# Performance work log

Hardware: AMD Instinct MI355X
Metric: run time of the kernel (lower is better)

Reference implementation:

```python
import jax, jax.numpy as jnp
import numpy as np

B, S, DIN, DH = 8, 4096, 1024, 1024


def setup_inputs() -> dict:
    key = jax.random.key(0)
    k1, k2, k3, k4 = jax.random.split(key, 4)
    x = jax.random.normal(k1, (B, S, DIN), jnp.float32)
    # previous hidden state must be strictly positive (log-domain scan)
    h = jax.random.uniform(k2, (B, 1, DH), jnp.float32, minval=0.05, maxval=0.95)
    W = jax.random.normal(k3, (2 * DH, DIN), jnp.float32) * (1.0 / np.sqrt(DIN))
    b = jax.random.normal(k4, (2 * DH,), jnp.float32) * 0.01
    return {"x": x, "h": h, "W": W, "b": b}


def _log_g(x):
    # log of g(x) = x + 0.5 if x >= 0 else sigmoid(x)
    return jnp.where(x >= 0, jnp.log(jnp.where(x >= 0, x, 0.0) + 0.5), -jax.nn.softplus(-x))


def reference(x, h, W, b):
    # gate/hidden projection: (B,S,2H)
    gh = jnp.einsum('bsi,oi->bso', x, W) + b
    gate, hidden = jnp.split(gh, 2, axis=2)  # each (B,S,H)

    # minGRU recurrence h_t = (1-z_t) h_{t-1} + z_t g(hidden_t), z_t = sigmoid(gate_t)
    # evaluated with the Heinsen log-space parallel scan
    log_z = -jax.nn.softplus(-gate)        # log sigmoid(gate)
    log_coeffs = -jax.nn.softplus(gate)    # log (1 - sigmoid(gate))
    log_h0 = jnp.log(h)                    # (B,1,H)
    log_values = jnp.concatenate([log_h0, log_z + _log_g(hidden)], axis=1)  # (B,S+1,H)

    a_star = jnp.cumsum(jnp.pad(log_coeffs, ((0, 0), (1, 0), (0, 0))), axis=1)  # (B,S+1,H)
    log_h = a_star + jax.lax.cumlogsumexp(log_values - a_star, axis=1)
    return jnp.exp(log_h)[:, 1:]  # (B,S,H)
```

## Files before the change

### kernel.cpp

```cpp
#include <hip/hip_runtime.h>

typedef __attribute__((ext_vector_type(4))) float f32x4;
typedef __attribute__((ext_vector_type(8))) short short8;

#define NCHUNK 64
#define CLEN 64

__device__ __forceinline__ unsigned short f2bf(float f) {
    union { float f; unsigned int u; } a; a.f = f;
    unsigned int r = a.u + 0x7fffu + ((a.u >> 16) & 1u);
    return (unsigned short)(r >> 16);
}
__device__ __forceinline__ float bf2f(unsigned short u) {
    union { unsigned int u; float f; } a; a.u = ((unsigned int)u) << 16;
    return a.f;
}

__global__ __launch_bounds__(256) void conv_all(const float* __restrict__ x,
                                                const float* __restrict__ W,
                                                unsigned short* __restrict__ xb,
                                                unsigned short* __restrict__ wbP) {
    int bid = blockIdx.x, t = threadIdx.x;
    if (bid < 2048) {
        for (int i = bid * 256 + t; i < 8388608; i += 524288) {
            float4 v = reinterpret_cast<const float4*>(x)[i];
            ushort4 o;
            o.x = f2bf(v.x); o.y = f2bf(v.y); o.z = f2bf(v.z); o.w = f2bf(v.w);
            reinterpret_cast<ushort4*>(xb)[i] = o;
        }
    } else {
        int base = (bid - 2048) * 256 + t;
#pragma unroll
        for (int k = 0; k < 4; ++k) {
            int i = base + k * 131072;
            int r = i >> 8, c4 = i & 255;
            float4 v = reinterpret_cast<const float4*>(W)[i];
            int rp;
            if (r < 1024) rp = (r >> 6) * 128 + (r & 63);
            else { int c = r - 1024; rp = (c >> 6) * 128 + 64 + (c & 63); }
            ushort4 o;
            o.x = f2bf(v.x); o.y = f2bf(v.y); o.z = f2bf(v.z); o.w = f2bf(v.w);
            reinterpret_cast<ushort4*>(wbP)[rp * 256 + c4] = o;
        }
    }
}

__global__ __launch_bounds__(256) void gemm_fused(
    const unsigned short* __restrict__ xb, const unsigned short* __restrict__ wbP,
    const float* __restrict__ bias,
    unsigned int* __restrict__ CVg, float* __restrict__ CCc, float* __restrict__ CVc)
{
    __shared__ unsigned short sm[16384];
    const int bid = blockIdx.x;
    const int swz = (bid & 7) * 512 + (bid >> 3);
    const int nt = swz & 15, mt = swz >> 4;
    const int m0 = mt * 128, chBase = nt * 64, n0p = nt * 128;
    const int t = threadIdx.x;
    const int w = t >> 6, l = t & 63;
    const int wr = (w >> 1) * 64, wc = (w & 1) * 64;

    const int srow = t >> 3;
    const int sblk = (t & 7) ^ (srow & 7);
    const unsigned short* gA = xb  + (size_t)(m0 + srow)  * 1024 + sblk * 8;
    const unsigned short* gB = wbP + (size_t)(n0p + srow) * 1024 + sblk * 8;

    f32x4 acc[4][4];
#pragma unroll
    for (int i = 0; i < 4; ++i)
#pragma unroll
        for (int j = 0; j < 4; ++j) acc[i][j] = (f32x4){0.f, 0.f, 0.f, 0.f};

    for (int kt = 0; kt < 16; ++kt) {
        __syncthreads();
        const unsigned short* a = gA + kt * 64;
        const unsigned short* b = gB + kt * 64;
#pragma unroll
        for (int j = 0; j < 4; ++j) {
            __builtin_amdgcn_global_load_lds(
                (const __attribute__((address_space(1))) unsigned int*)(a + j * 32768),
                (__attribute__((address_space(3))) unsigned int*)
                    ((__attribute__((address_space(3))) char*)sm + t * 16 + j * 4096), 16, 0, 0);
            __builtin_amdgcn_global_load_lds(
                (const __attribute__((address_space(1))) unsigned int*)(b + j * 32768),
                (__attribute__((address_space(3))) unsigned int*)
                    ((__attribute__((address_space(3))) char*)sm + 16384 + t * 16 + j * 4096), 16, 0, 0);
        }
        asm volatile("s_waitcnt vmcnt(0)" ::: "memory");
        __syncthreads();

#pragma unroll
        for (int ks = 0; ks < 2; ++ks) {
            short8 af[4], bfr[4];
#pragma unroll
            for (int mi = 0; mi < 4; ++mi) {
                int row = wr + mi * 16 + (l & 15);
                int slot = ((ks << 2) + (l >> 4)) ^ (l & 7);
                af[mi] = *reinterpret_cast<const short8*>((const char*)sm + row * 128 + slot * 16);
            }
#pragma unroll
            for (int ni = 0; ni < 4; ++ni) {
                int row = wc + ni * 16 + (l & 15);
                int slot = ((ks << 2) + (l >> 4)) ^ (l & 7);
                bfr[ni] = *reinterpret_cast<const short8*>((const char*)sm + 16384 + row * 128 + slot * 16);
            }
#pragma unroll
            for (int mi = 0; mi < 4; ++mi)
#pragma unroll
                for (int ni = 0; ni < 4; ++ni)
                    acc[mi][ni] = __builtin_amdgcn_mfma_f32_16x16x32_bf16(af[mi], bfr[ni], acc[mi][ni], 0, 0, 0);
        }
    }

    const bool isHid = (wc != 0);
    float bv[4];
#pragma unroll
    for (int ni = 0; ni < 4; ++ni) {
        int ch = chBase + ni * 16 + (l & 15);
        bv[ni] = bias[isHid ? (1024 + ch) : ch];
    }
    __syncthreads();
    {
        unsigned short* eb = sm + (w >> 1) * 8192 + (isHid ? 4096 : 0);
#pragma unroll
        for (int mi = 0; mi < 4; ++mi)
#pragma unroll
            for (int ni = 0; ni < 4; ++ni)
#pragma unroll
                for (int r = 0; r < 4; ++r) {
                    float v = acc[mi][ni][r] + bv[ni];
                    float o = isHid ? ((v >= 0.f) ? (v + 0.5f) : (1.f / (1.f + __expf(-v))))
                                    : (1.f / (1.f + __expf(-v)));
                    int row = mi * 16 + ((l >> 4) << 2) + r;
                    int ch = ni * 16 + (l & 15);
                    eb[row * 64 + ch] = f2bf(o);
                }
    }
    __syncthreads();
    {
        int chunk = t >> 7, tt = t & 127;
        const unsigned short* zb = sm + chunk * 8192;
        const unsigned short* gb = zb + 4096;
        int mrow0 = m0 + chunk * 64;
#pragma unroll 4
        for (int i = 0; i < 32; ++i) {
            int idx = i * 128 + tt;
            int row = idx >> 6, ch = idx & 63;
            float z = bf2f(zb[row * 64 + ch]);
            float gg = bf2f(gb[row * 64 + ch]);
            CVg[(size_t)(mrow0 + row) * 1024 + chBase + ch] =
                (unsigned int)f2bf(1.f - z) | ((unsigned int)f2bf(z * gg) << 16);
        }
        if (tt < 64) {
            float C = 1.f, V = 0.f;
#pragma unroll 8
            for (int i = 0; i < 64; ++i) {
                float z = bf2f(zb[i * 64 + tt]);
                float gg = bf2f(gb[i * 64 + tt]);
                float c = bf2f(f2bf(1.f - z));
                float vv = bf2f(f2bf(z * gg));
                C *= c; V = c * V + vv;
            }
            int b = mrow0 >> 12, ck = (mrow0 >> 6) & 63;
            CCc[(size_t)(b * 64 + ck) * 1024 + chBase + tt] = C;
            CVc[(size_t)(b * 64 + ck) * 1024 + chBase + tt] = V;
        }
    }
}

__global__ __launch_bounds__(256) void scan_prefix(
    const float* __restrict__ CC, const float* __restrict__ CV,
    const float* __restrict__ h0, float* __restrict__ Hinit)
{
    int g = blockIdx.x * 256 + threadIdx.x;
    int h = g & 1023, b = g >> 10;
    float hc = h0[b * 1024 + h];
#pragma unroll 8
    for (int ck = 0; ck < NCHUNK; ++ck) {
        int idx = (b * 64 + ck) * 1024 + h;
        Hinit[idx] = hc;
        hc = CC[idx] * hc + CV[idx];
    }
}

__global__ __launch_bounds__(256) void scan_apply(
    const unsigned int* __restrict__ CVg, const float* __restrict__ Hinit,
    float* __restrict__ out)
{
    int g = blockIdx.x * 256 + threadIdx.x;
    int ch = g & 1023, ck = (g >> 10) & 63, b = g >> 16;
    int mbase = b * 4096 + ck * CLEN;
    const unsigned int* pc = CVg + (size_t)mbase * 1024 + ch;
    float h = Hinit[g];
    float* po = out + (size_t)mbase * 1024 + ch;
#pragma unroll 8
    for (int i = 0; i < CLEN; ++i) {
        unsigned int u = pc[i * 1024];
        h = bf2f((unsigned short)(u & 0xffff)) * h + bf2f((unsigned short)(u >> 16));
        po[i * 1024] = h;
    }
}

extern "C" void kernel_launch(void* const* d_in, const int* in_sizes, int n_in,
                              void* d_out, int out_size, void* d_ws, size_t ws_size,
                              hipStream_t stream)
{
    const float* x    = (const float*)d_in[0];
    const float* h0   = (const float*)d_in[1];
    const float* W    = (const float*)d_in[2];
    const float* bias = (const float*)d_in[3];
    float* out = (float*)d_out;

    unsigned short* xb = (unsigned short*)d_out;
    unsigned short* wbP = (unsigned short*)d_ws;
    unsigned int* CVg = (unsigned int*)((char*)d_ws + 4194304);
    float* CCc   = (float*)((char*)d_ws + 138412032);
    float* CVc   = (float*)((char*)d_ws + 140509184);
    float* Hinit = (float*)((char*)d_ws + 142606336);

    conv_all<<<2560, 256, 0, stream>>>(x, W, xb, wbP);
    gemm_fused<<<4096, 256, 0, stream>>>(xb, wbP, bias, CVg, CCc, CVc);
    scan_prefix<<<32, 256, 0, stream>>>(CCc, CVc, h0, Hinit);
    scan_apply<<<2048, 256, 0, stream>>>(CVg, Hinit, out);
}
```

Before: 488.8 us.

## Triple-buffer GEMM K-loop with async LDS prefetch and fuse scan kernels

The GEMM main loop now uses a three-stage LDS ring with K-tiles of 32. The next-but-one tile is issued via global_load_lds while the current tile is consumed, with partial vmcnt waits and one barrier per iteration. MFMA issue is wrapped in setprio, which should overlap memory latency with compute instead of a full load-wait-compute cycle. Separately, the serial scan_prefix kernel is removed: each scan_all thread recomputes its chunk's initial state from the chunk carries. That saves a launch and the Hinit round trip, but adds redundant serial work for later chunks.

```diff
diff --git a/kernel.cpp b/kernel.cpp
--- a/kernel.cpp
+++ b/kernel.cpp
@@ -45,12 +45,26 @@
     }
 }
 
+
+#define GLOAD(SRC, DST) \
+    __builtin_amdgcn_global_load_lds((const __attribute__((address_space(1))) unsigned int*)(SRC), \
+        (__attribute__((address_space(3))) unsigned int*)(DST), 16, 0, 0)
+
+#define STAGE(KT, BUF) { \
+    const unsigned short* _a = gA + (KT) * 32; \
+    const unsigned short* _b = gB + (KT) * 32; \
+    char* _dA = lds + (BUF) * 8192 + t * 16; \
+    char* _dB = lds + 24576 + (BUF) * 8192 + t * 16; \
+    GLOAD(_a, _dA); GLOAD(_a + 65536, _dA + 4096); \
+    GLOAD(_b, _dB); GLOAD(_b + 65536, _dB + 4096); }
+
 __global__ __launch_bounds__(256) void gemm_fused(
     const unsigned short* __restrict__ xb, const unsigned short* __restrict__ wbP,
     const float* __restrict__ bias,
     unsigned int* __restrict__ CVg, float* __restrict__ CCc, float* __restrict__ CVc)
 {
-    __shared__ unsigned short sm[16384];
+    __shared__ char lds[49152];
+    unsigned short* sm = (unsigned short*)lds;
     const int bid = blockIdx.x;
     const int swz = (bid & 7) * 512 + (bid >> 3);
     const int nt = swz & 15, mt = swz >> 4;
@@ -59,56 +73,51 @@
     const int w = t >> 6, l = t & 63;
     const int wr = (w >> 1) * 64, wc = (w & 1) * 64;
 
-    const int srow = t >> 3;
-    const int sblk = (t & 7) ^ (srow & 7);
+    const int srow = t >> 2;
+    const int sblk = (t & 3) ^ ((t >> 3) & 3);
     const unsigned short* gA = xb  + (size_t)(m0 + srow)  * 1024 + sblk * 8;
     const unsigned short* gB = wbP + (size_t)(n0p + srow) * 1024 + sblk * 8;
 
+    const int rslot = ((l >> 4) ^ ((l >> 1) & 3)) * 16;
+    const int aoff = (wr + (l & 15)) * 64 + rslot;
+    const int boff = (wc + (l & 15)) * 64 + rslot;
+
     f32x4 acc[4][4];
 #pragma unroll
     for (int i = 0; i < 4; ++i)
 #pragma unroll
         for (int j = 0; j < 4; ++j) acc[i][j] = (f32x4){0.f, 0.f, 0.f, 0.f};
 
-    for (int kt = 0; kt < 16; ++kt) {
-        __syncthreads();
-        const unsigned short* a = gA + kt * 64;
-        const unsigned short* b = gB + kt * 64;
-#pragma unroll
-        for (int j = 0; j < 4; ++j) {
-            __builtin_amdgcn_global_load_lds(
-                (const __attribute__((address_space(1))) unsigned int*)(a + j * 32768),
-                (__attribute__((address_space(3))) unsigned int*)
-                    ((__attribute__((address_space(3))) char*)sm + t * 16 + j * 4096), 16, 0, 0);
-            __builtin_amdgcn_global_load_lds(
-                (const __attribute__((address_space(1))) unsigned int*)(b + j * 32768),
-                (__attribute__((address_space(3))) unsigned int*)
-                    ((__attribute__((address_space(3))) char*)sm + 16384 + t * 16 + j * 4096), 16, 0, 0);
-        }
-        asm volatile("s_waitcnt vmcnt(0)" ::: "memory");
-        __syncthreads();
-
-#pragma unroll
-        for (int ks = 0; ks < 2; ++ks) {
-            short8 af[4], bfr[4];
-#pragma unroll
-            for (int mi = 0; mi < 4; ++mi) {
-                int row = wr + mi * 16 + (l & 15);
-                int slot = ((ks << 2) + (l >> 4)) ^ (l & 7);
-                af[mi] = *reinterpret_cast<const short8*>((const char*)sm + row * 128 + slot * 16);
-            }
-#pragma unroll
-            for (int ni = 0; ni < 4; ++ni) {
-                int row = wc + ni * 16 + (l & 15);
-                int slot = ((ks << 2) + (l >> 4)) ^ (l & 7);
-                bfr[ni] = *reinterpret_cast<const short8*>((const char*)sm + 16384 + row * 128 + slot * 16);
-            }
-#pragma unroll
-            for (int mi = 0; mi < 4; ++mi)
-#pragma unroll
-                for (int ni = 0; ni < 4; ++ni)
-                    acc[mi][ni] = __builtin_amdgcn_mfma_f32_16x16x32_bf16(af[mi], bfr[ni], acc[mi][ni], 0, 0, 0);
-        }
+    STAGE(0, 0); STAGE(1, 1);
+    asm volatile("s_waitcnt vmcnt(4)" ::: "memory");
+    __builtin_amdgcn_sched_barrier(0);
+    __builtin_amdgcn_s_barrier();
+
+    int rb = 0, wb = 2;
+    for (int kt = 0; kt < 32; ++kt) {
+        if (kt < 30) STAGE(kt + 2, wb);
+        const char* bA = lds + rb * 8192;
+        const char* bB = lds + 24576 + rb * 8192;
+        short8 af[4], bfr[4];
+#pragma unroll
+        for (int mi = 0; mi < 4; ++mi) af[mi]  = *reinterpret_cast<const short8*>(bA + aoff + mi * 1024);
+#pragma unroll
+        for (int ni = 0; ni < 4; ++ni) bfr[ni] = *reinterpret_cast<const short8*>(bB + boff + ni * 1024);
+        asm volatile("s_waitcnt lgkmcnt(0)" ::: "memory");
+        __builtin_amdgcn_sched_barrier(0);
+        __builtin_amdgcn_s_setprio(1);
+#pragma unroll
+        for (int mi = 0; mi < 4; ++mi)
+#pragma unroll
+            for (int ni = 0; ni < 4; ++ni)
+                acc[mi][ni] = __builtin_amdgcn_mfma_f32_16x16x32_bf16(af[mi], bfr[ni], acc[mi][ni], 0, 0, 0);
+        __builtin_amdgcn_s_setprio(0);
+        __builtin_amdgcn_sched_barrier(0);
+        if (kt < 30)       { asm volatile("s_waitcnt vmcnt(4)" ::: "memory"); }
+        else if (kt == 30) { asm volatile("s_waitcnt vmcnt(0)" ::: "memory"); }
+        __builtin_amdgcn_s_barrier();
+        rb = (rb == 2) ? 0 : rb + 1;
+        wb = (wb == 2) ? 0 : wb + 1;
     }
 
     const bool isHid = (wc != 0);
@@ -167,34 +176,24 @@
     }
 }
 
-__global__ __launch_bounds__(256) void scan_prefix(
-    const float* __restrict__ CC, const float* __restrict__ CV,
-    const float* __restrict__ h0, float* __restrict__ Hinit)
-{
-    int g = blockIdx.x * 256 + threadIdx.x;
-    int h = g & 1023, b = g >> 10;
-    float hc = h0[b * 1024 + h];
-#pragma unroll 8
-    for (int ck = 0; ck < NCHUNK; ++ck) {
-        int idx = (b * 64 + ck) * 1024 + h;
-        Hinit[idx] = hc;
-        hc = CC[idx] * hc + CV[idx];
-    }
-}
-
-__global__ __launch_bounds__(256) void scan_apply(
-    const unsigned int* __restrict__ CVg, const float* __restrict__ Hinit,
-    float* __restrict__ out)
+__global__ __launch_bounds__(256) void scan_all(
+    const unsigned int* __restrict__ CVg, const float* __restrict__ CC,
+    const float* __restrict__ CV, const float* __restrict__ h0, float* __restrict__ out)
 {
     int g = blockIdx.x * 256 + threadIdx.x;
     int ch = g & 1023, ck = (g >> 10) & 63, b = g >> 16;
+    float h = h0[b * 1024 + ch];
+    const float* pc = CC + (size_t)b * 65536 + ch;
+    const float* pv = CV + (size_t)b * 65536 + ch;
+#pragma unroll 4
+    for (int k = 0; k < ck; ++k)
+        h = pc[k * 1024] * h + pv[k * 1024];
     int mbase = b * 4096 + ck * CLEN;
-    const unsigned int* pc = CVg + (size_t)mbase * 1024 + ch;
-    float h = Hinit[g];
+    const unsigned int* p = CVg + (size_t)mbase * 1024 + ch;
     float* po = out + (size_t)mbase * 1024 + ch;
 #pragma unroll 8
     for (int i = 0; i < CLEN; ++i) {
-        unsigned int u = pc[i * 1024];
+        unsigned int u = p[i * 1024];
         h = bf2f((unsigned short)(u & 0xffff)) * h + bf2f((unsigned short)(u >> 16));
         po[i * 1024] = h;
     }
@@ -213,12 +212,10 @@
     unsigned short* xb = (unsigned short*)d_out;
     unsigned short* wbP = (unsigned short*)d_ws;
     unsigned int* CVg = (unsigned int*)((char*)d_ws + 4194304);
-    float* CCc   = (float*)((char*)d_ws + 138412032);
-    float* CVc   = (float*)((char*)d_ws + 140509184);
-    float* Hinit = (float*)((char*)d_ws + 142606336);
+    float* CCc = (float*)((char*)d_ws + 138412032);
+    float* CVc = (float*)((char*)d_ws + 140509184);
 
     conv_all<<<2560, 256, 0, stream>>>(x, W, xb, wbP);
     gemm_fused<<<4096, 256, 0, stream>>>(xb, wbP, bias, CVg, CCc, CVc);
-    scan_prefix<<<32, 256, 0, stream>>>(CCc, CVc, h0, Hinit);
-    scan_apply<<<2048, 256, 0, stream>>>(CVg, Hinit, out);
-}
+    scan_all<<<2048, 256, 0, stream>>>(CVg, CCc, CVc, h0, out);
+}
```

New measurement: 464.4 us. -5.0%, faster.
